# Kernel optimization log

Hardware: AMD Instinct MI355X
Metric: run time of the kernel (lower is better)

## Reference

```python
import jax, jax.numpy as jnp
import numpy as np

B, N_CH, T, E = 64, 64, 1000, 512
KS = [3, 5, 7]
TC, AH, GC, HEADS, NCLS = 16, 32, 32, 4, 2
F3 = TC * len(KS)
EPS = 1e-5


def _gat(x, src, dst, W, a_src, a_dst, bias, N):
    # PyG GATConv, concat=False: h = x @ W.T -> [N, H, C]
    H, C = a_src.shape
    h = (x @ W.T).reshape(-1, H, C)
    al_s = (h * a_src).sum(-1)  # [N, H]
    al_d = (h * a_dst).sum(-1)
    e = al_s[src] + al_d[dst]  # [E, H]
    e = jnp.where(e > 0, e, 0.2 * e)  # leaky_relu(0.2)
    emax = jax.ops.segment_max(e, dst, num_segments=N)
    ex = jnp.exp(e - emax[dst])
    denom = jax.ops.segment_sum(ex, dst, num_segments=N)
    alpha = ex / denom[dst]
    out = jax.ops.segment_sum(h[src] * alpha[:, :, None], dst, num_segments=N)
    return out.mean(1) + bias  # concat=False -> head mean, then bias


def _branch(xr, cw, cb, g, b, m, v, w1, b1, w2, b2):
    k = cw.shape[-1]
    o = jax.lax.conv_general_dilated(xr, cw, (1,), [(k // 2, k // 2)],
                                     dimension_numbers=('NCH', 'OIH', 'NCH'))
    o = o + cb[None, :, None]
    o = (o - m[None, :, None]) / jnp.sqrt(v[None, :, None] + EPS) * g[None, :, None] + b[None, :, None]
    o = jax.nn.gelu(o, approximate=False)
    h = jnp.tanh(jnp.einsum('hc,nct->nht', w1, o) + b1[None, :, None])
    s = jnp.einsum('oh,nht->not', w2, h) + b2[None, :, None]  # [N,1,T]
    wts = jax.nn.softmax(s, axis=2)
    return (o * wts).sum(-1)  # [N, TC]


def reference(x, edge_index,
              conv_w_0, conv_b_0, bn_g_0, bn_b_0, bn_m_0, bn_v_0, aw1_0, ab1_0, aw2_0, ab2_0,
              conv_w_1, conv_b_1, bn_g_1, bn_b_1, bn_m_1, bn_v_1, aw1_1, ab1_1, aw2_1, ab2_1,
              conv_w_2, conv_b_2, bn_g_2, bn_b_2, bn_m_2, bn_v_2, aw1_2, ab1_2, aw2_2, ab2_2,
              se_w1, se_b1, se_w2, se_b2,
              gat1_w, gat1_asrc, gat1_adst, gat1_bias, bn1_g, bn1_b, bn1_m, bn1_v,
              skip_w, skip_b,
              gat2_w, gat2_asrc, gat2_adst, gat2_bias, bn2_g, bn2_b, bn2_m, bn2_v,
              fc_w, fc_b):
    Bx, n, Tn = x.shape
    xr = x.reshape(Bx * n, 1, Tn)
    branches = [
        (conv_w_0, conv_b_0, bn_g_0, bn_b_0, bn_m_0, bn_v_0, aw1_0, ab1_0, aw2_0, ab2_0),
        (conv_w_1, conv_b_1, bn_g_1, bn_b_1, bn_m_1, bn_v_1, aw1_1, ab1_1, aw2_1, ab2_1),
        (conv_w_2, conv_b_2, bn_g_2, bn_b_2, bn_m_2, bn_v_2, aw1_2, ab1_2, aw2_2, ab2_2),
    ]
    feats = [_branch(xr, *p) for p in branches]
    xf = jnp.concatenate(feats, axis=1)  # [B*n, F3]
    # SE block (squeeze over all nodes, per original mean over dim 0)
    sq = xf.mean(0, keepdims=True)
    sq = jax.nn.gelu(sq @ se_w1.T + se_b1, approximate=False)
    sq = jax.nn.sigmoid(sq @ se_w2.T + se_b2)
    xf = xf * sq
    # batched edge index + self loops (PyG GATConv default add_self_loops)
    offs = (jnp.arange(Bx) * n).astype(edge_index.dtype)
    src = (edge_index[0][None, :] + offs[:, None]).reshape(-1)
    dst = (edge_index[1][None, :] + offs[:, None]).reshape(-1)
    loops = jnp.arange(Bx * n, dtype=edge_index.dtype)
    src = jnp.concatenate([src, loops])
    dst = jnp.concatenate([dst, loops])
    Nn = Bx * n
    h1 = _gat(xf, src, dst, gat1_w, gat1_asrc, gat1_adst, gat1_bias, Nn)
    h1 = (h1 - bn1_m) / jnp.sqrt(bn1_v + EPS) * bn1_g + bn1_b
    h1 = jax.nn.gelu(h1 + xf @ skip_w.T + skip_b, approximate=False)
    h2 = _gat(h1, src, dst, gat2_w, gat2_asrc, gat2_adst, gat2_bias, Nn)
    h2 = (h2 - bn2_m) / jnp.sqrt(bn2_v + EPS) * bn2_g + bn2_b
    h2 = jax.nn.gelu(h2 + h1, approximate=False)
    pooled = h2.reshape(Bx, n, -1).mean(1)  # global_mean_pool per graph
    return pooled @ fc_w.T + fc_b


def setup_inputs() -> dict:
    key = jax.random.key(0)
    it = iter(jax.random.split(key, 80))
    nk = lambda *s: jax.random.normal(next(it), s, jnp.float32) * 0.1
    d = {}
    d['x'] = jax.random.normal(next(it), (B, N_CH, T), jnp.float32)
    s0 = jax.random.randint(next(it), (E,), 0, N_CH)
    off = jax.random.randint(next(it), (E,), 1, N_CH)
    d['edge_index'] = jnp.stack([s0, (s0 + off) % N_CH]).astype(jnp.int32)  # no self loops
    for i, k in enumerate(KS):
        d[f'conv_w_{i}'] = nk(TC, 1, k); d[f'conv_b_{i}'] = nk(TC)
        d[f'bn_g_{i}'] = 1.0 + nk(TC); d[f'bn_b_{i}'] = nk(TC)
        d[f'bn_m_{i}'] = nk(TC); d[f'bn_v_{i}'] = 1.0 + jnp.abs(nk(TC))
        d[f'aw1_{i}'] = nk(AH, TC); d[f'ab1_{i}'] = nk(AH)
        d[f'aw2_{i}'] = nk(1, AH); d[f'ab2_{i}'] = nk(1)
    d['se_w1'] = nk(F3 // 4, F3); d['se_b1'] = nk(F3 // 4)
    d['se_w2'] = nk(F3, F3 // 4); d['se_b2'] = nk(F3)
    d['gat1_w'] = nk(HEADS * GC, F3)
    d['gat1_asrc'] = nk(HEADS, GC); d['gat1_adst'] = nk(HEADS, GC); d['gat1_bias'] = nk(GC)
    d['bn1_g'] = 1.0 + nk(GC); d['bn1_b'] = nk(GC); d['bn1_m'] = nk(GC); d['bn1_v'] = 1.0 + jnp.abs(nk(GC))
    d['skip_w'] = nk(GC, F3); d['skip_b'] = nk(GC)
    d['gat2_w'] = nk(HEADS * GC, GC)
    d['gat2_asrc'] = nk(HEADS, GC); d['gat2_adst'] = nk(HEADS, GC); d['gat2_bias'] = nk(GC)
    d['bn2_g'] = 1.0 + nk(GC); d['bn2_b'] = nk(GC); d['bn2_m'] = nk(GC); d['bn2_v'] = 1.0 + jnp.abs(nk(GC))
    d['fc_w'] = nk(NCLS, GC); d['fc_b'] = nk(NCLS)
    return d
```

## Files before the change

### kernel.cpp

```cpp
#include <hip/hip_runtime.h>
#include <math.h>

#define N_NODES 4096
#define T_LEN 1000
#define TCH 16
#define AHD 32
#define F3D 48
#define GCD 32
#define NPG 64
#define NGRAPH 64
#define BN_EPS 1e-5f

typedef _Float16 half4_t __attribute__((ext_vector_type(4)));
typedef float float4_t __attribute__((ext_vector_type(4)));

__device__ __forceinline__ float fast_rcp(float x){ return __builtin_amdgcn_rcpf(x); }
__device__ __forceinline__ float gelu_exact(float v){
    return 0.5f*v*(1.0f+erff(v*0.70710678118654752f));
}

struct BranchParams {
    const float* conv_w; const float* conv_b;
    const float* bn_g; const float* bn_b; const float* bn_m; const float* bn_v;
    const float* aw1; const float* ab1; const float* aw2; const float* ab2;
    int K; int col0;
};

__global__ __launch_bounds__(256)
void branch_kernel(const float* __restrict__ x,
                   BranchParams bp0, BranchParams bp1, BranchParams bp2,
                   float* __restrict__ xf, float* __restrict__ colacc)
{
    __shared__ __align__(16) float xs_f[1056];
    __shared__ __align__(8)  _Float16 xsc[4][1048];
    __shared__ __align__(8)  _Float16 cws16[256];
    __shared__ float s_arr[1024];
    __shared__ __align__(16) float shiftc[16];
    __shared__ float scl[16];
    __shared__ float reds[4];
    __shared__ __align__(16) float fredw[4][16];

    const BranchParams bp = (blockIdx.y==0)? bp0 : (blockIdx.y==1)? bp1 : bp2;
    const int tid = threadIdx.x;
    const int node = blockIdx.x;
    const int K = bp.K;
    const float* xrow = x + (size_t)node*T_LEN;

    for (int j=tid;j<1056;j+=256){
        int q = j-8;
        xs_f[j] = (q>=0 && q<T_LEN)? xrow[q] : 0.f;
    }
    if (tid<16){
        float s = bp.bn_g[tid]*rsqrtf(bp.bn_v[tid]+BN_EPS);
        scl[tid]=s;
        shiftc[tid] = (bp.conv_b[tid]-bp.bn_m[tid])*s + bp.bn_b[tid];
    }
    __syncthreads();
    for (int j=tid;j<1048;j+=256){
        xsc[0][j]=(_Float16)xs_f[j];
        xsc[1][j]=(_Float16)xs_f[j+1];
        xsc[2][j]=(_Float16)xs_f[j+2];
        xsc[3][j]=(_Float16)xs_f[j+3];
    }
    {
        int ch=tid>>4, tap=tid&15;
        cws16[tid] = (tap<K)? (_Float16)(bp.conv_w[ch*K+tap]*scl[ch]) : (_Float16)0.f;
    }
    __syncthreads();

    const int lane = tid&63, wave = tid>>6;
    const int col  = lane&15;
    const int kg   = (lane>>4)<<2;

    const half4_t  acw = *(const half4_t*)&cws16[col*16+kg];
    const float4_t csh = *(const float4_t*)&shiftc[kg];

    const float TWO_LOG2E = 2.8853900817779268f;
    const float LOG2E = 1.4426950408889634f;

    float4_t wr0 = *(const float4_t*)&bp.aw1[(size_t)col*TCH + kg];
    float4_t wr1 = *(const float4_t*)&bp.aw1[(size_t)(col+16)*TCH + kg];
    half4_t a0,a1;
    #pragma unroll
    for (int r=0;r<4;r++){ a0[r]=(_Float16)(wr0[r]*TWO_LOG2E); a1[r]=(_Float16)(wr1[r]*TWO_LOG2E); }
    float4_t c0  = *(const float4_t*)&bp.ab1[kg];
    float4_t c1  = *(const float4_t*)&bp.ab1[16+kg];
    #pragma unroll
    for (int r=0;r<4;r++){ c0[r]*=TWO_LOG2E; c1[r]*=TWO_LOG2E; }
    float4_t w20 = *(const float4_t*)&bp.aw2[kg];
    float4_t w21 = *(const float4_t*)&bp.aw2[16+kg];
    #pragma unroll
    for (int r=0;r<4;r++){ w20[r]*=LOG2E; w21[r]*=LOG2E; }
    const float b2v = bp.ab2[0]*LOG2E;
    const float w2sum8 = w20[0]+w20[1]+w20[2]+w20[3]+w21[0]+w21[1]+w21[2]+w21[3];

    const float C1GE = -2.30220818f;
    const float C2GE = -0.10294324f;

    const int abase = 8 + wave*256 + col + kg - K/2;
    const int sh = abase & 3;
    const _Float16* xw_base = &xsc[sh][abase - sh];

    half4_t oreg[16];
    #pragma unroll
    for (int i=0;i<16;i++){
        half4_t xw = *(const half4_t*)(xw_base + i*16);
        float4_t d = __builtin_amdgcn_mfma_f32_16x16x16f16(acw, xw, csh, 0,0,0);

        float vv[4], dd[4];
        #pragma unroll
        for (int r=0;r<4;r++){
            float v = d[r];
            vv[r] = v;
            float t = fmaxf(v, -9.0f);
            float u = t*t;
            float pq = fmaf(C2GE, u, C1GE);
            dd[r] = __builtin_amdgcn_exp2f(pq*t) + 1.0f;
        }
        half4_t ob;
        {
            float rp0 = fast_rcp(dd[0]*dd[1]);
            float rp1 = fast_rcp(dd[2]*dd[3]);
            ob[0] = (_Float16)(vv[0]*(dd[1]*rp0));
            ob[1] = (_Float16)(vv[1]*(dd[0]*rp0));
            ob[2] = (_Float16)(vv[2]*(dd[3]*rp1));
            ob[3] = (_Float16)(vv[3]*(dd[2]*rp1));
        }
        oreg[i] = ob;

        float4_t h0 = __builtin_amdgcn_mfma_f32_16x16x16f16(a0, ob, c0, 0,0,0);
        float4_t h1 = __builtin_amdgcn_mfma_f32_16x16x16f16(a1, ob, c1, 0,0,0);
        float accr = 0.f;
        #pragma unroll
        for (int r=0;r<4;r++){
            float e0 = __builtin_amdgcn_exp2f(h0[r]) + 1.0f;
            float e1 = __builtin_amdgcn_exp2f(h1[r]) + 1.0f;
            float rp = fast_rcp(e0*e1);
            accr = fmaf(w20[r], e1*rp, accr);
            accr = fmaf(w21[r], e0*rp, accr);
        }
        float part = fmaf(-2.0f, accr, w2sum8);
        part += __shfl_xor(part,16);
        part += __shfl_xor(part,32);
        const int pos0 = wave*256 + i*16;
        if (lane<16) s_arr[pos0+lane] = (pos0+lane < T_LEN)? (part + b2v) : -INFINITY;
    }
    __syncthreads();

    float sv[4];
    #pragma unroll
    for (int ii=0;ii<4;ii++) sv[ii]=s_arr[tid+ii*256];
    float e[4]; float ls=0.f;
    #pragma unroll
    for (int ii=0;ii<4;ii++){ e[ii]=__builtin_amdgcn_exp2f(sv[ii]); ls+=e[ii]; }
    #pragma unroll
    for (int off=32;off;off>>=1) ls += __shfl_xor(ls,off);
    if (lane==0) reds[wave]=ls;
    __syncthreads();
    const float invS = fast_rcp(reds[0]+reds[1]+reds[2]+reds[3]);
    #pragma unroll
    for (int ii=0;ii<4;ii++) s_arr[tid+ii*256]=e[ii];
    __syncthreads();

    half4_t acch = {(_Float16)0.f,(_Float16)0.f,(_Float16)0.f,(_Float16)0.f};
    #pragma unroll
    for (int i=0;i<16;i++){
        _Float16 eh = (_Float16)s_arr[wave*256 + i*16 + col];
        half4_t evv = {eh,eh,eh,eh};
        acch += oreg[i]*evv;
    }
    {
        union { half4_t h; unsigned u[2]; } au, bu;
        au.h = acch;
        #pragma unroll
        for (int off=1;off<16;off<<=1){
            bu.u[0] = __shfl_xor(au.u[0], off);
            bu.u[1] = __shfl_xor(au.u[1], off);
            au.h += bu.h;
        }
        if (col==0){
            float4_t accf;
            #pragma unroll
            for (int r=0;r<4;r++) accf[r] = (float)au.h[r];
            *(float4_t*)&fredw[wave][kg] = accf;
        }
    }
    __syncthreads();
    if (tid<16){
        float v = (fredw[0][tid]+fredw[1][tid]+fredw[2][tid]+fredw[3][tid])*invS;
        xf[(size_t)node*F3D + bp.col0 + tid] = v;
        atomicAdd(&colacc[bp.col0 + tid], v);
    }
}

__global__ __launch_bounds__(128)
void csr_local_kernel(const int* __restrict__ ei, int epg,
                      int* __restrict__ rowstart, int* __restrict__ cols){
    __shared__ int deg[64], cur[64], rs[65];
    const int tid = threadIdx.x;
    if (tid<64) deg[tid]=0;
    __syncthreads();
    const int total = epg + 64;
    for (int e=tid;e<total;e+=128){
        int d = (e<epg)? ei[epg+e] : (e-epg);
        atomicAdd(&deg[d],1);
    }
    __syncthreads();
    if (tid<64){
        int v = deg[tid];
        int s = v;
        #pragma unroll
        for (int off=1;off<64;off<<=1){
            int t = __shfl_up(s, off);
            if (tid >= off) s += t;
        }
        rs[tid+1] = s;
        if (tid==0) rs[0]=0;
        cur[tid] = s - v;
    }
    __syncthreads();
    for (int e=tid;e<total;e+=128){
        int sN,dN;
        if (e<epg){ sN=ei[e]; dN=ei[epg+e]; } else { sN=dN=e-epg; }
        int pos = atomicAdd(&cur[dN],1);
        cols[pos]=sN;
    }
    if (tid<65) rowstart[tid]=rs[tid];
}

__global__ __launch_bounds__(128)
void gat_h1_kernel(const float* __restrict__ xf, const float* __restrict__ colacc,
                   const float* __restrict__ se_w1, const float* __restrict__ se_b1,
                   const float* __restrict__ se_w2, const float* __restrict__ se_b2,
                   const float* __restrict__ W,
                   const float* __restrict__ a_src, const float* __restrict__ a_dst,
                   float* __restrict__ hbuf, float* __restrict__ als, float* __restrict__ ald){
    __shared__ float cm[F3D];
    __shared__ float g1[12];
    __shared__ float xin[F3D];
    __shared__ float hs[128];
    const int node=blockIdx.x, tid=threadIdx.x;
    if (tid<F3D) cm[tid]=colacc[tid]*(1.0f/(float)N_NODES);
    __syncthreads();
    if (tid<12){
        float v=se_b1[tid];
        for (int j=0;j<F3D;j++) v += se_w1[tid*F3D+j]*cm[j];
        g1[tid]=gelu_exact(v);
    }
    __syncthreads();
    if (tid<F3D){
        float v=se_b2[tid];
        for (int m2=0;m2<12;m2++) v += se_w2[tid*12+m2]*g1[m2];
        xin[tid] = xf[(size_t)node*F3D+tid]*fast_rcp(1.0f+__expf(-v));
    }
    __syncthreads();
    float acc=0.f;
    const float* wr = W + (size_t)tid*F3D;
    #pragma unroll
    for (int j=0;j<F3D;j++) acc += wr[j]*xin[j];
    hs[tid]=acc;
    hbuf[(size_t)node*128+tid]=acc;
    __syncthreads();
    if (tid<8){
        int head=tid&3;
        const float* av = (tid<4)? a_src : a_dst;
        float s=0.f;
        for (int c=0;c<GCD;c++) s += hs[head*GCD+c]*av[head*GCD+c];
        if (tid<4) als[(size_t)node*4+head]=s;
        else       ald[(size_t)node*4+head]=s;
    }
}

__global__ __launch_bounds__(512)
void gat_tail_kernel(const int* __restrict__ rowstart, const int* __restrict__ cols,
                     const float* __restrict__ als, const float* __restrict__ ald,
                     const float* __restrict__ hbuf,
                     const float* __restrict__ bias1,
                     const float* __restrict__ bn1_g, const float* __restrict__ bn1_b,
                     const float* __restrict__ bn1_m, const float* __restrict__ bn1_v,
                     const float* __restrict__ xf, const float* __restrict__ colacc,
                     const float* __restrict__ se_w1, const float* __restrict__ se_b1,
                     const float* __restrict__ se_w2, const float* __restrict__ se_b2,
                     const float* __restrict__ skip_w, const float* __restrict__ skip_b,
                     const float* __restrict__ W2,
                     const float* __restrict__ asrc2, const float* __restrict__ adst2,
                     const float* __restrict__ bias2,
                     const float* __restrict__ bn2_g, const float* __restrict__ bn2_b,
                     const float* __restrict__ bn2_m, const float* __restrict__ bn2_v,
                     const float* __restrict__ fc_w, const float* __restrict__ fc_b,
                     float* __restrict__ out)
{
    __shared__ float hb[64*128];
    __shared__ float xh[64*48];
    __shared__ float h1l[64*32];
    __shared__ float a1s[256], a1d[256], a2s[256], a2d[256];
    __shared__ float skw[32*48];
    __shared__ float poolv[32];
    __shared__ float cm[F3D], g1[12], gate_sh[F3D];

    const int g = blockIdx.x;
    const int tid = threadIdx.x;
    const int n0 = g*NPG;

    if (tid<F3D) cm[tid]=colacc[tid]*(1.0f/(float)N_NODES);
    __syncthreads();
    if (tid<12){
        float v=se_b1[tid];
        for (int j=0;j<F3D;j++) v += se_w1[tid*F3D+j]*cm[j];
        g1[tid]=gelu_exact(v);
    }
    __syncthreads();
    if (tid<F3D){
        float v=se_b2[tid];
        for (int m2=0;m2<12;m2++) v += se_w2[tid*12+m2]*g1[m2];
        gate_sh[tid]=fast_rcp(1.0f+__expf(-v));
    }
    __syncthreads();

    for (int i=tid;i<64*128;i+=512) hb[i] = hbuf[(size_t)n0*128 + i];
    for (int i=tid;i<64*48;i+=512)  xh[i] = xf[(size_t)n0*F3D + i] * gate_sh[i%F3D];
    for (int i=tid;i<32*48;i+=512)  skw[i] = skip_w[i];
    if (tid<256){ a1s[tid]=als[n0*4+tid]; a1d[tid]=ald[n0*4+tid]; }
    __syncthreads();

    for (int p=0;p<4;p++){
        const int nl = p*16 + (tid>>5);
        const int c  = tid&31;
        const float4 ad = *(const float4*)&a1d[nl*4];
        float m0=0,m1=0,m2=0,m3=0,d0=0,d1=0,d2=0,d3=0;
        const int s0=rowstart[nl], s1=rowstart[nl+1];
        for (int e=s0;e<s1;e++){
            const int sl = cols[e];
            const float4 as=*(const float4*)&a1s[sl*4];
            float e0=as.x+ad.x; e0=e0>0.f?e0:0.2f*e0; float w0=__expf(e0);
            float e1=as.y+ad.y; e1=e1>0.f?e1:0.2f*e1; float w1=__expf(e1);
            float e2=as.z+ad.z; e2=e2>0.f?e2:0.2f*e2; float w2=__expf(e2);
            float e3=as.w+ad.w; e3=e3>0.f?e3:0.2f*e3; float w3=__expf(e3);
            const float* hr=&hb[sl*128];
            m0+=w0*hr[c]; m1+=w1*hr[32+c]; m2+=w2*hr[64+c]; m3+=w3*hr[96+c];
            d0+=w0; d1+=w1; d2+=w2; d3+=w3;
        }
        float acc = 0.25f*(m0*fast_rcp(d0)+m1*fast_rcp(d1)+m2*fast_rcp(d2)+m3*fast_rcp(d3)) + bias1[c];
        acc = (acc-bn1_m[c])*rsqrtf(bn1_v[c]+BN_EPS)*bn1_g[c]+bn1_b[c];
        float sk = skip_b[c];
        const float* xr=&xh[nl*F3D];
        #pragma unroll
        for (int j=0;j<F3D;j++) sk += xr[j]*skw[c*F3D+j];
        h1l[nl*32+c]=gelu_exact(acc+sk);
    }
    __syncthreads();

    for (int i=tid;i<64*128;i+=512){
        const int nl=i>>7, r=i&127;
        const float4* h1r=(const float4*)&h1l[nl*32];
        const float4* wr =(const float4*)&W2[r*32];
        float acc=0.f;
        #pragma unroll
        for (int j=0;j<8;j++){
            float4 a=h1r[j], b=wr[j];
            acc += a.x*b.x + a.y*b.y + a.z*b.z + a.w*b.w;
        }
        hb[i]=acc;
    }
    __syncthreads();

    {
        const int which = tid>>8;
        const int idx = tid&255;
        const int nl=idx>>2, h=idx&3;
        const float* av = which? &adst2[h*32] : &asrc2[h*32];
        const float* hr = &hb[nl*128 + h*32];
        float s=0.f;
        #pragma unroll
        for (int c=0;c<32;c++) s += hr[c]*av[c];
        if (which) a2d[idx]=s; else a2s[idx]=s;
    }
    __syncthreads();

    for (int p=0;p<4;p++){
        const int nl = p*16 + (tid>>5);
        const int c  = tid&31;
        const float4 ad = *(const float4*)&a2d[nl*4];
        float m0=0,m1=0,m2=0,m3=0,d0=0,d1=0,d2=0,d3=0;
        const int s0=rowstart[nl], s1=rowstart[nl+1];
        for (int e=s0;e<s1;e++){
            const int sl = cols[e];
            const float4 as=*(const float4*)&a2s[sl*4];
            float e0=as.x+ad.x; e0=e0>0.f?e0:0.2f*e0; float w0=__expf(e0);
            float e1=as.y+ad.y; e1=e1>0.f?e1:0.2f*e1; float w1=__expf(e1);
            float e2=as.z+ad.z; e2=e2>0.f?e2:0.2f*e2; float w2=__expf(e2);
            float e3=as.w+ad.w; e3=e3>0.f?e3:0.2f*e3; float w3=__expf(e3);
            const float* hr=&hb[sl*128];
            m0+=w0*hr[c]; m1+=w1*hr[32+c]; m2+=w2*hr[64+c]; m3+=w3*hr[96+c];
            d0+=w0; d1+=w1; d2+=w2; d3+=w3;
        }
        float acc = 0.25f*(m0*fast_rcp(d0)+m1*fast_rcp(d1)+m2*fast_rcp(d2)+m3*fast_rcp(d3)) + bias2[c];
        acc = (acc-bn2_m[c])*rsqrtf(bn2_v[c]+BN_EPS)*bn2_g[c]+bn2_b[c];
        float v = acc + h1l[nl*32+c];
        xh[nl*32+c]=gelu_exact(v);
    }
    __syncthreads();

    if (tid<32){
        float s=0.f;
        for (int n=0;n<NPG;n++) s += xh[n*32+tid];
        poolv[tid]=s*(1.0f/(float)NPG);
    }
    __syncthreads();
    if (tid<2){
        float o=fc_b[tid];
        #pragma unroll
        for (int c=0;c<GCD;c++) o += poolv[c]*fc_w[tid*GCD+c];
        out[g*2+tid]=o;
    }
}

extern "C" void kernel_launch(void* const* d_in, const int* in_sizes, int n_in,
                              void* d_out, int out_size, void* d_ws, size_t ws_size,
                              hipStream_t stream){
    const float* x = (const float*)d_in[0];
    const int* ei = (const int*)d_in[1];
    const int epg = in_sizes[1]/2;

    float* ws = (float*)d_ws;
    float* xf      = ws;
    float* colacc  = xf + (size_t)N_NODES*F3D;
    float* hbuf    = colacc + 64;
    float* als     = hbuf + (size_t)N_NODES*128;
    float* ald     = als + (size_t)N_NODES*4;
    int*   rowstart = (int*)(ald + (size_t)N_NODES*4);
    int*   cols     = rowstart + 80;

    auto P = [&](int i){ return (const float*)d_in[i]; };

    (void)hipMemsetAsync(colacc, 0, 64*sizeof(float), stream);
    csr_local_kernel<<<1,128,0,stream>>>(ei,epg,rowstart,cols);

    BranchParams bps[3];
    const int Ks[3] = {3,5,7};
    for (int b=0;b<3;b++){
        int base = 2 + b*10;
        bps[b].conv_w = P(base+0); bps[b].conv_b = P(base+1);
        bps[b].bn_g = P(base+2);   bps[b].bn_b = P(base+3);
        bps[b].bn_m = P(base+4);   bps[b].bn_v = P(base+5);
        bps[b].aw1 = P(base+6);    bps[b].ab1 = P(base+7);
        bps[b].aw2 = P(base+8);    bps[b].ab2 = P(base+9);
        bps[b].K = Ks[b]; bps[b].col0 = b*TCH;
    }
    branch_kernel<<<dim3(N_NODES,3),256,0,stream>>>(x, bps[0], bps[1], bps[2], xf, colacc);

    gat_h1_kernel<<<N_NODES,128,0,stream>>>(xf,colacc,P(32),P(33),P(34),P(35),
                                            P(36),P(37),P(38),hbuf,als,ald);

    gat_tail_kernel<<<NGRAPH,512,0,stream>>>(
        rowstart,cols,als,ald,hbuf,
        P(39),P(40),P(41),P(42),P(43),
        xf,colacc,P(32),P(33),P(34),P(35),
        P(44),P(45),
        P(46),P(47),P(48),P(49),P(50),P(51),P(52),P(53),
        P(54),P(55),(float*)d_out);
}
```

Baseline: 238.3 us.

## Fuse GAT layer-1 projection and attention logits into the per-graph tail kernel

Removes the separate per-node gat_h1_kernel and computes the x@W1 projection and the source/destination attention scores inside gat_tail_kernel, directly into shared memory for each graph's 64 nodes. This drops one kernel launch and the global round trip of hbuf/als/ald, along with the per-node recomputation of the SE gate. In exchange, the projection now runs on only 64 blocks instead of 4096, so parallelism for that stage is much lower.

Result: faster. 232.0 us, median of 2 (-2.6%).

```diff
diff --git a/kernel.cpp b/kernel.cpp
--- a/kernel.cpp
+++ b/kernel.cpp
@@ -228,59 +228,16 @@
     if (tid<65) rowstart[tid]=rs[tid];
 }
 
-__global__ __launch_bounds__(128)
-void gat_h1_kernel(const float* __restrict__ xf, const float* __restrict__ colacc,
-                   const float* __restrict__ se_w1, const float* __restrict__ se_b1,
-                   const float* __restrict__ se_w2, const float* __restrict__ se_b2,
-                   const float* __restrict__ W,
-                   const float* __restrict__ a_src, const float* __restrict__ a_dst,
-                   float* __restrict__ hbuf, float* __restrict__ als, float* __restrict__ ald){
-    __shared__ float cm[F3D];
-    __shared__ float g1[12];
-    __shared__ float xin[F3D];
-    __shared__ float hs[128];
-    const int node=blockIdx.x, tid=threadIdx.x;
-    if (tid<F3D) cm[tid]=colacc[tid]*(1.0f/(float)N_NODES);
-    __syncthreads();
-    if (tid<12){
-        float v=se_b1[tid];
-        for (int j=0;j<F3D;j++) v += se_w1[tid*F3D+j]*cm[j];
-        g1[tid]=gelu_exact(v);
-    }
-    __syncthreads();
-    if (tid<F3D){
-        float v=se_b2[tid];
-        for (int m2=0;m2<12;m2++) v += se_w2[tid*12+m2]*g1[m2];
-        xin[tid] = xf[(size_t)node*F3D+tid]*fast_rcp(1.0f+__expf(-v));
-    }
-    __syncthreads();
-    float acc=0.f;
-    const float* wr = W + (size_t)tid*F3D;
-    #pragma unroll
-    for (int j=0;j<F3D;j++) acc += wr[j]*xin[j];
-    hs[tid]=acc;
-    hbuf[(size_t)node*128+tid]=acc;
-    __syncthreads();
-    if (tid<8){
-        int head=tid&3;
-        const float* av = (tid<4)? a_src : a_dst;
-        float s=0.f;
-        for (int c=0;c<GCD;c++) s += hs[head*GCD+c]*av[head*GCD+c];
-        if (tid<4) als[(size_t)node*4+head]=s;
-        else       ald[(size_t)node*4+head]=s;
-    }
-}
-
 __global__ __launch_bounds__(512)
 void gat_tail_kernel(const int* __restrict__ rowstart, const int* __restrict__ cols,
-                     const float* __restrict__ als, const float* __restrict__ ald,
-                     const float* __restrict__ hbuf,
+                     const float* __restrict__ xf, const float* __restrict__ colacc,
+                     const float* __restrict__ se_w1, const float* __restrict__ se_b1,
+                     const float* __restrict__ se_w2, const float* __restrict__ se_b2,
+                     const float* __restrict__ W1,
+                     const float* __restrict__ asrc1, const float* __restrict__ adst1,
                      const float* __restrict__ bias1,
                      const float* __restrict__ bn1_g, const float* __restrict__ bn1_b,
                      const float* __restrict__ bn1_m, const float* __restrict__ bn1_v,
-                     const float* __restrict__ xf, const float* __restrict__ colacc,
-                     const float* __restrict__ se_w1, const float* __restrict__ se_b1,
-                     const float* __restrict__ se_w2, const float* __restrict__ se_b2,
                      const float* __restrict__ skip_w, const float* __restrict__ skip_b,
                      const float* __restrict__ W2,
                      const float* __restrict__ asrc2, const float* __restrict__ adst2,
@@ -317,10 +274,35 @@
     }
     __syncthreads();
 
-    for (int i=tid;i<64*128;i+=512) hb[i] = hbuf[(size_t)n0*128 + i];
     for (int i=tid;i<64*48;i+=512)  xh[i] = xf[(size_t)n0*F3D + i] * gate_sh[i%F3D];
     for (int i=tid;i<32*48;i+=512)  skw[i] = skip_w[i];
-    if (tid<256){ a1s[tid]=als[n0*4+tid]; a1d[tid]=ald[n0*4+tid]; }
+    __syncthreads();
+
+    for (int i=tid;i<64*128;i+=512){
+        const int nl=i>>7, r=i&127;
+        const float4* xr=(const float4*)&xh[nl*48];
+        const float4* wr=(const float4*)&W1[r*48];
+        float acc=0.f;
+        #pragma unroll
+        for (int j=0;j<12;j++){
+            float4 a=xr[j], b=wr[j];
+            acc += a.x*b.x + a.y*b.y + a.z*b.z + a.w*b.w;
+        }
+        hb[i]=acc;
+    }
+    __syncthreads();
+
+    {
+        const int which = tid>>8;
+        const int idx = tid&255;
+        const int nl=idx>>2, h=idx&3;
+        const float* av = which? &adst1[h*32] : &asrc1[h*32];
+        const float* hr = &hb[nl*128 + h*32];
+        float s=0.f;
+        #pragma unroll
+        for (int c=0;c<32;c++) s += hr[c]*av[c];
+        if (which) a1d[idx]=s; else a1s[idx]=s;
+    }
     __syncthreads();
 
     for (int p=0;p<4;p++){
@@ -425,10 +407,7 @@
     float* ws = (float*)d_ws;
     float* xf      = ws;
     float* colacc  = xf + (size_t)N_NODES*F3D;
-    float* hbuf    = colacc + 64;
-    float* als     = hbuf + (size_t)N_NODES*128;
-    float* ald     = als + (size_t)N_NODES*4;
-    int*   rowstart = (int*)(ald + (size_t)N_NODES*4);
+    int*   rowstart = (int*)(colacc + 64);
     int*   cols     = rowstart + 80;
 
     auto P = [&](int i){ return (const float*)d_in[i]; };
@@ -449,13 +428,11 @@
     }
     branch_kernel<<<dim3(N_NODES,3),256,0,stream>>>(x, bps[0], bps[1], bps[2], xf, colacc);
 
-    gat_h1_kernel<<<N_NODES,128,0,stream>>>(xf,colacc,P(32),P(33),P(34),P(35),
-                                            P(36),P(37),P(38),hbuf,als,ald);
-
     gat_tail_kernel<<<NGRAPH,512,0,stream>>>(
-        rowstart,cols,als,ald,hbuf,
+        rowstart,cols,
+        xf,colacc,P(32),P(33),P(34),P(35),
+        P(36),P(37),P(38),
         P(39),P(40),P(41),P(42),P(43),
-        xf,colacc,P(32),P(33),P(34),P(35),
         P(44),P(45),
         P(46),P(47),P(48),P(49),P(50),P(51),P(52),P(53),
         P(54),P(55),(float*)d_out);
```
